# Optimization experiments

Measured on AMD Instinct MI355X. Metric: run time of the kernel, lower is better.

The kernel has to match this reference:

```python
import jax, jax.numpy as jnp
import numpy as np

J, C, F, K = 4096, 8192, 64, 2  # jobs, total nodes, out feats, TAGConv hops (DGL default K=2)


def setup_inputs() -> dict:
    key = jax.random.key(0)
    ks = jax.random.split(key, 8)
    h = jax.random.uniform(ks[0], (J,), jnp.float32)
    L = jax.random.uniform(ks[1], (J,), jnp.float32)
    W = jax.random.uniform(ks[2], (), jnp.float32)
    P = jax.random.uniform(ks[3], (), jnp.float32)
    N = jax.random.uniform(ks[4], (), jnp.float32)
    Graph = jax.random.randint(ks[5], (J, C), 0, 2).astype(jnp.float32)
    tag_w = jax.random.normal(ks[6], ((K + 1) * 6, F), jnp.float32) * 0.05  # TAGConv lin weight on concat of K+1 hops
    tag_b = jnp.zeros((F,), jnp.float32)
    lin_w = jax.random.normal(ks[7], (F, C), jnp.float32) * 0.05
    lin_b = jnp.zeros((C,), jnp.float32)
    return dict(h=h, L=L, W=W, P=P, N=N, Graph=Graph,
                tag_w=tag_w, tag_b=tag_b, lin_w=lin_w, lin_b=lin_b)


def _mask(Graph):
    Jn, Cn = Graph.shape
    row = Graph.sum(axis=1, keepdims=True)          # [J,1]
    col = Graph.sum(axis=0, keepdims=True)          # [1,C]
    colJ = col[:, :Jn]                               # [1,J]
    left = 1.0 - row - row.T - colJ - colJ.T         # [J,J]
    left = jnp.where(left == 1.0, 1.0, 0.0)
    left = jnp.triu(left, k=1)
    right = 1.0 - jnp.broadcast_to(row, (Jn, Cn - Jn))
    return jnp.concatenate([left, right], axis=1)    # [J,C]


def reference(h, L, W, P, N, Graph, tag_w, tag_b, lin_w, lin_b):
    Jn, Cn = Graph.shape
    # sort jobs by h descending, pair with L
    order = jnp.argsort(-h)
    jobList = jnp.stack([h[order], L[order]], axis=1)                 # [J,2]
    other = jnp.stack([W, P, N, jnp.asarray(1.0, h.dtype)])           # [4]
    X = jnp.concatenate([jobList, jnp.broadcast_to(other, (Jn, 4))], axis=1)  # [J,6]
    X = jnp.concatenate([X, jnp.zeros((Cn - Jn, 6), X.dtype)], axis=0)        # [C,6]
    # pad adjacency to square CxC
    A = jnp.concatenate([Graph, jnp.zeros((Cn - Jn, Cn), Graph.dtype)], axis=0)
    # DGL TAGConv: norm = clamp(in_deg,1)^-0.5; edge i->j iff A[i,j]==1 => aggregate = A^T @ x
    deg = A.sum(axis=0)
    norm = jnp.clip(deg, 1.0) ** -0.5

    def prop(x):
        return (A.T @ (x * norm[:, None])) * norm[:, None]

    f0 = X
    f1 = prop(f0)
    f2 = prop(f1)
    G_t = jnp.concatenate([f0, f1, f2], axis=1) @ tag_w + tag_b       # [C,F]
    Value = G_t[:Jn] @ lin_w + lin_b                                   # [J,C]
    tmp = Value - (1.0 - _mask(Graph)) * 10000.0
    Poss = jax.nn.softmax(tmp.reshape(-1)).reshape(tmp.shape)
    return (Value, Poss)
```

## Files before the change

kernel.cpp:

```cpp
#include <hip/hip_runtime.h>
#include <math.h>

#define JN 4096
#define CN 8192

typedef __attribute__((ext_vector_type(8))) short short8;
typedef __attribute__((ext_vector_type(4))) float f32x4;

#define WS_LWT    0
#define WS_GTB    262144
#define WS_ROWSUM 393216
#define WS_DEG    397312
#define WS_NORM   401408
#define WS_X      405504
#define WS_F1     430080
#define WS_PART   454656

#define PS_BITR    0
#define PS_COLPART 524288
#define PS_P1      589824
#define PS_P2      983040

__device__ __forceinline__ unsigned short f2bf(float x) {
    unsigned int u = __float_as_uint(x);
    u += 0x7fffu + ((u >> 16) & 1u);
    return (unsigned short)(u >> 16);
}

__device__ __forceinline__ float gt_val(const float* __restrict__ x, const float* __restrict__ a,
                                        const float* __restrict__ b, const float* __restrict__ tw,
                                        float acc, int f) {
#pragma unroll
    for (int k = 0; k < 6; ++k) acc += x[k] * tw[k * 64 + f];
#pragma unroll
    for (int k = 0; k < 6; ++k) acc += a[k] * tw[(k + 6) * 64 + f];
#pragma unroll
    for (int k = 0; k < 6; ++k) acc += b[k] * tw[(k + 12) * 64 + f];
    return acc;
}

__global__ __launch_bounds__(256) void k_front(const float* __restrict__ G,
                                               const float* __restrict__ h, const float* __restrict__ L,
                                               const float* __restrict__ Wp, const float* __restrict__ Pp,
                                               const float* __restrict__ Np,
                                               const float* __restrict__ lw,
                                               float* __restrict__ rowsum,
                                               unsigned long long* __restrict__ bitR,
                                               float* __restrict__ X,
                                               unsigned short* __restrict__ lwT) {
    __shared__ float redf[4];
    __shared__ int redi[4];
    __shared__ float s_t[64][65];
    int wv = threadIdx.x >> 6, lane = threadIdx.x & 63;
    if (blockIdx.x < JN) {
        int row = blockIdx.x;
        const f32x4* g4 = (const f32x4*)(G + (size_t)row * CN);
        unsigned long long* brow = bitR + (size_t)row * 64;
        float s = 0.f;
#pragma unroll
        for (int i = 0; i < 4; ++i) {
            f32x4 v = __builtin_nontemporal_load(&g4[i * 256 + wv * 64 + lane]);
            s += v[0] + v[1] + v[2] + v[3];
            unsigned long long b0 = __ballot(v[0] != 0.f);
            unsigned long long b1 = __ballot(v[1] != 0.f);
            unsigned long long b2 = __ballot(v[2] != 0.f);
            unsigned long long b3 = __ballot(v[3] != 0.f);
            if (!lane) {
                int base = i * 16 + wv * 4;
                brow[base] = b0; brow[base + 1] = b1; brow[base + 2] = b2; brow[base + 3] = b3;
            }
        }
#pragma unroll
        for (int i = 4; i < 8; ++i) {
            f32x4 v = __builtin_nontemporal_load(&g4[i * 256 + wv * 64 + lane]);
            s += v[0] + v[1] + v[2] + v[3];
        }
        for (int o = 32; o; o >>= 1) s += __shfl_down(s, o, 64);
        if (!lane) redf[wv] = s;
        __syncthreads();
        if (!threadIdx.x) rowsum[row] = redf[0] + redf[1] + redf[2] + redf[3];
    } else if (blockIdx.x < 2 * JN) {
        int i = blockIdx.x - JN;
        float hi = h[i];
        int cnt = 0;
        for (int j = threadIdx.x; j < JN; j += 256) {
            float hj = h[j];
            cnt += (hj > hi) || (hj == hi && j < i);
        }
        for (int o = 32; o; o >>= 1) cnt += __shfl_down(cnt, o, 64);
        if (!lane) redi[wv] = cnt;
        __syncthreads();
        if (!threadIdx.x) {
            int r = redi[0] + redi[1] + redi[2] + redi[3];
            float* xr = X + r * 6;
            xr[0] = hi; xr[1] = L[i]; xr[2] = *Wp; xr[3] = *Pp; xr[4] = *Np; xr[5] = 1.f;
        }
    } else {
        int c0 = (blockIdx.x - 2 * JN) * 64;
        for (int t = threadIdx.x; t < 4096; t += 256) {
            int f = t >> 6, cc = t & 63;
            s_t[f][cc] = lw[(size_t)f * CN + c0 + cc];
        }
        __syncthreads();
        for (int q = threadIdx.x; q < 512; q += 256) {
            int c = q >> 3, kc = q & 7;
            short8 pack;
#pragma unroll
            for (int i = 0; i < 8; ++i) pack[i] = (short)f2bf(s_t[kc * 8 + i][c]);
            *(short8*)(lwT + ((size_t)(c0 + c)) * 64 + kc * 8) = pack;
        }
    }
}

__global__ __launch_bounds__(256) void k_colsum_bits(const unsigned long long* __restrict__ bitR,
                                                     float* __restrict__ colpart) {
    __shared__ unsigned long long s_bits[256][4];
    int bx = blockIdx.x, r0 = blockIdx.y * 256;
    int tid = threadIdx.x;
    for (int t = tid; t < 1024; t += 256) {
        int r = t >> 2, wl = t & 3;
        s_bits[r][wl] = bitR[(size_t)(r0 + r) * 64 + bx * 4 + wl];
    }
    __syncthreads();
    int wl = tid & 3, bit = tid >> 2;
    int cnt = 0;
    for (int r = 0; r < 256; ++r)
        cnt += (int)((s_bits[r][wl] >> bit) & 1ull);
    colpart[(size_t)blockIdx.y * JN + bx * 256 + tid] = (float)cnt;
}

__global__ __launch_bounds__(256) void k_prop1(const unsigned long long* __restrict__ bitR,
                                               const float* __restrict__ X,
                                               const float* __restrict__ colpart,
                                               float* __restrict__ deg, float* __restrict__ norm,
                                               float* __restrict__ part) {
    __shared__ unsigned long long s_bits[256][4];
    __shared__ float s_in[256 * 6];
    __shared__ float s_norm[256];
    int bx = blockIdx.x, r0 = blockIdx.y * 256;
    int tid = threadIdx.x;
    {
        float d = 0.f;
        for (int ch = 0; ch < 16; ++ch) d += colpart[(size_t)ch * JN + r0 + tid];
        float dc = d < 1.f ? 1.f : d;
        float nv = rsqrtf(dc);
        s_norm[tid] = nv;
        if (bx == 0) { deg[r0 + tid] = d; norm[r0 + tid] = nv; }
    }
    for (int t = tid; t < 1024; t += 256) {
        int r = t >> 2, wl = t & 3;
        s_bits[r][wl] = bitR[(size_t)(r0 + r) * 64 + bx * 4 + wl];
    }
    __syncthreads();
    for (int t = tid; t < 1536; t += 256)
        s_in[t] = X[r0 * 6 + t] * s_norm[t / 6];
    __syncthreads();
    int wl = tid & 3, bit = tid >> 2;
    float a0 = 0, a1 = 0, a2 = 0, a3 = 0, a4 = 0, a5 = 0;
    for (int r = 0; r < 256; ++r) {
        float g = (float)((s_bits[r][wl] >> bit) & 1ull);
        const float* x = &s_in[r * 6];
        a0 += g * x[0]; a1 += g * x[1]; a2 += g * x[2];
        a3 += g * x[3]; a4 += g * x[4]; a5 += g * x[5];
    }
    float* o = part + ((size_t)blockIdx.y * JN + bx * 256 + tid) * 6;
    o[0] = a0; o[1] = a1; o[2] = a2; o[3] = a3; o[4] = a4; o[5] = a5;
}

__global__ __launch_bounds__(256) void k_prop2(const unsigned long long* __restrict__ bitR,
                                               const float* __restrict__ p1, const float* __restrict__ norm,
                                               float* __restrict__ f1, float* __restrict__ part) {
    __shared__ unsigned long long s_bits[256][4];
    __shared__ float s_in[256 * 6];
    int bx = blockIdx.x, r0 = blockIdx.y * 256;
    int tid = threadIdx.x;
    for (int t = tid; t < 1024; t += 256) {
        int r = t >> 2, wl = t & 3;
        s_bits[r][wl] = bitR[(size_t)(r0 + r) * 64 + bx * 4 + wl];
    }
    for (int t = tid; t < 1536; t += 256) {
        float s = 0.f;
        for (int ch = 0; ch < 16; ++ch) s += p1[(size_t)ch * 24576 + r0 * 6 + t];
        int row = r0 + t / 6;
        float n = norm[row];
        float f1v = s * n;
        if (bx == 0) f1[r0 * 6 + t] = f1v;
        s_in[t] = f1v * n;
    }
    __syncthreads();
    int wl = tid & 3, bit = tid >> 2;
    float a0 = 0, a1 = 0, a2 = 0, a3 = 0, a4 = 0, a5 = 0;
    for (int r = 0; r < 256; ++r) {
        float g = (float)((s_bits[r][wl] >> bit) & 1ull);
        const float* x = &s_in[r * 6];
        a0 += g * x[0]; a1 += g * x[1]; a2 += g * x[2];
        a3 += g * x[3]; a4 += g * x[4]; a5 += g * x[5];
    }
    float* o = part + ((size_t)blockIdx.y * JN + bx * 256 + tid) * 6;
    o[0] = a0; o[1] = a1; o[2] = a2; o[3] = a3; o[4] = a4; o[5] = a5;
}

__global__ __launch_bounds__(256) void k_gt(const float* __restrict__ p2, const float* __restrict__ norm,
                                            const float* __restrict__ f1, const float* __restrict__ X,
                                            const float* __restrict__ tw, const float* __restrict__ tb,
                                            unsigned short* __restrict__ Gtb) {
    __shared__ float s_x[64 * 6], s_f1[64 * 6], s_f2[64 * 6];
    __shared__ float s_tw[18 * 64], s_tb[64];
    int j0 = blockIdx.x * 64, tid = threadIdx.x;
    for (int t = tid; t < 1152; t += 256) s_tw[t] = tw[t];
    if (tid < 64) s_tb[tid] = tb[tid];
    for (int t = tid; t < 384; t += 256) {
        s_x[t] = X[j0 * 6 + t];
        s_f1[t] = f1[j0 * 6 + t];
        float s = 0.f;
        for (int ch = 0; ch < 16; ++ch) s += p2[(size_t)ch * 24576 + j0 * 6 + t];
        s_f2[t] = s * norm[j0 + t / 6];
    }
    __syncthreads();
    int row = tid & 63, fg = tid >> 6;
    float xv[6], av[6], bv[6];
#pragma unroll
    for (int k = 0; k < 6; ++k) {
        xv[k] = s_x[row * 6 + k]; av[k] = s_f1[row * 6 + k]; bv[k] = s_f2[row * 6 + k];
    }
    short8 p0, p1v;
#pragma unroll
    for (int i = 0; i < 16; ++i) {
        int f = fg * 16 + i;
        float acc = gt_val(xv, av, bv, s_tw, s_tb[f], f);
        unsigned short u = f2bf(acc);
        if (i < 8) p0[i] = (short)u; else p1v[i - 8] = (short)u;
    }
    *(short8*)(Gtb + (size_t)(j0 + row) * 64 + fg * 16) = p0;
    *(short8*)(Gtb + (size_t)(j0 + row) * 64 + fg * 16 + 8) = p1v;
}

#define GEMM_PROLOGUE()                                                                   \
    __shared__ unsigned short sGt[64 * 64];                                               \
    __shared__ unsigned short sW[256 * 64];                                               \
    int j0 = blockIdx.y * 64, c0 = blockIdx.x * 256, tid = threadIdx.x;                   \
    for (int q = tid; q < 2048; q += 256) {                                               \
        int col = q >> 3, off = q & 7;                                                    \
        short8 v = *(const short8*)(lwT + ((size_t)(c0 + col)) * 64 + off * 8);           \
        int byte = (col * 128 + off * 16) ^ ((col & 7) << 4);                             \
        *(short8*)((char*)sW + byte) = v;                                                 \
    }                                                                                     \
    for (int q = tid; q < 512; q += 256) {                                                \
        int row = q >> 3, off = q & 7;                                                    \
        short8 v = *(const short8*)(Gtb + ((size_t)(j0 + row)) * 64 + off * 8);           \
        int byte = (row * 128 + off * 16) ^ ((row & 7) << 4);                             \
        *(short8*)((char*)sGt + byte) = v;                                                \
    }                                                                                     \
    __syncthreads();                                                                      \
    int lane = tid & 63, w = tid >> 6;                                                    \
    int lrow = lane & 15, kg = lane >> 4;                                                 \
    f32x4 acc[4][4];                                            \
    for (int m = 0; m < 4; ++m)                                                           \
        for (int n = 0; n < 4; ++n) acc[m][n] = (f32x4){0.f, 0.f, 0.f, 0.f};              \
    for (int ks = 0; ks < 2; ++ks) {                                                      \
        int kb = ks * 64 + kg * 16;                                                       \
        short8 wf[4], gf[4];                                                              \
        for (int m = 0; m < 4; ++m) {                                                     \
            int col = w * 64 + m * 16 + lrow;                                             \
            wf[m] = *(const short8*)((const char*)sW + ((col * 128 + kb) ^ ((col & 7) << 4))); \
        }                                                                                 \
        for (int n = 0; n < 4; ++n) {                                                     \
            int row = n * 16 + lrow;                                                      \
            gf[n] = *(const short8*)((const char*)sGt + ((row * 128 + kb) ^ ((row & 7) << 4))); \
        }                                                                                 \
        for (int m = 0; m < 4; ++m)                                                       \
            for (int n = 0; n < 4; ++n)                                                   \
                acc[m][n] = __builtin_amdgcn_mfma_f32_16x16x32_bf16(wf[m], gf[n], acc[m][n], 0, 0, 0); \
    }                                                                                     \
    bool left = (c0 < JN);                                                                \
    int cb[4]; f32x4 lb4[4], rsc4[4], dgc4[4];                                            \
    for (int m = 0; m < 4; ++m) {                                                         \
        cb[m] = c0 + w * 64 + m * 16 + kg * 4;                                            \
        lb4[m] = *(const f32x4*)&lb[cb[m]];                                               \
        if (left) { rsc4[m] = *(const f32x4*)&rowsum[cb[m]]; dgc4[m] = *(const f32x4*)&deg[cb[m]]; } \
        else      { rsc4[m] = (f32x4){0,0,0,0}; dgc4[m] = (f32x4){0,0,0,0}; }             \
    }

__global__ __launch_bounds__(256) void k_valueA(const unsigned short* __restrict__ Gtb,
                                                const unsigned short* __restrict__ lwT,
                                                const float* __restrict__ lb,
                                                const float* __restrict__ rowsum, const float* __restrict__ deg,
                                                float* __restrict__ Value, float* __restrict__ partials) {
    GEMM_PROLOGUE()
    __shared__ float sRedM[4], sRedS[4];

    float mx = -INFINITY;
#pragma unroll
    for (int n = 0; n < 4; ++n) {
        int j = j0 + n * 16 + lrow;
        float rs_i = rowsum[j], dg_i = deg[j];
#pragma unroll
        for (int m = 0; m < 4; ++m) {
            f32x4 v4 = acc[m][n] + lb4[m];
            __builtin_nontemporal_store(v4, (f32x4*)&Value[(size_t)j * CN + cb[m]]);
            f32x4 t4;
#pragma unroll
            for (int u = 0; u < 4; ++u) {
                float om;
                if (left) {
                    bool m1 = ((rs_i + rsc4[m][u] + dg_i + dgc4[m][u]) == 0.0f) && (cb[m] + u > j);
                    om = m1 ? 0.f : 1.f;
                } else {
                    om = rs_i;
                }
                t4[u] = v4[u] - om * 10000.f;
            }
            acc[m][n] = t4;
            mx = fmaxf(fmaxf(fmaxf(mx, t4[0]), t4[1]), fmaxf(t4[2], t4[3]));
        }
    }
    float sm = 0.f;
#pragma unroll
    for (int n = 0; n < 4; ++n)
#pragma unroll
        for (int m = 0; m < 4; ++m)
#pragma unroll
            for (int u = 0; u < 4; ++u) sm += __expf(acc[m][n][u] - mx);

    for (int o = 32; o; o >>= 1) {
        float om_ = __shfl_down(mx, o, 64);
        float os_ = __shfl_down(sm, o, 64);
        float nm = fmaxf(mx, om_);
        sm = sm * __expf(mx - nm) + os_ * __expf(om_ - nm);
        mx = nm;
    }
    if (!lane) { sRedM[w] = mx; sRedS[w] = sm; }
    __syncthreads();
    if (!tid) {
        float M = sRedM[0], S = sRedS[0];
        for (int i = 1; i < 4; ++i) {
            float nm = fmaxf(M, sRedM[i]);
            S = S * __expf(M - nm) + sRedS[i] * __expf(sRedM[i] - nm);
            M = nm;
        }
        int bid = blockIdx.y * gridDim.x + blockIdx.x;
        partials[2 * bid] = M;
        partials[2 * bid + 1] = S;
    }
}

__global__ __launch_bounds__(256) void k_valueB(const unsigned short* __restrict__ Gtb,
                                                const unsigned short* __restrict__ lwT,
                                                const float* __restrict__ lb,
                                                const float* __restrict__ rowsum, const float* __restrict__ deg,
                                                const float* __restrict__ partials, float* __restrict__ Poss) {
    __shared__ float sRedM[4], sRedS[4], sG[2];
    {
        int tid0 = threadIdx.x;
        float mx = -INFINITY, sm = 0.f;
        for (int i = tid0; i < 2048; i += 256) {
            float m = partials[2 * i], s = partials[2 * i + 1];
            float nm = fmaxf(mx, m);
            sm = sm * __expf(mx - nm) + s * __expf(m - nm);
            mx = nm;
        }
        for (int o = 32; o; o >>= 1) {
            float om_ = __shfl_down(mx, o, 64);
            float os_ = __shfl_down(sm, o, 64);
            float nm = fmaxf(mx, om_);
            sm = sm * __expf(mx - nm) + os_ * __expf(om_ - nm);
            mx = nm;
        }
        int lane0 = tid0 & 63, w0 = tid0 >> 6;
        if (!lane0) { sRedM[w0] = mx; sRedS[w0] = sm; }
        __syncthreads();
        if (!tid0) {
            float M = sRedM[0], S = sRedS[0];
            for (int i = 1; i < 4; ++i) {
                float nm = fmaxf(M, sRedM[i]);
                S = S * __expf(M - nm) + sRedS[i] * __expf(sRedM[i] - nm);
                M = nm;
            }
            sG[0] = M; sG[1] = S;
        }
        __syncthreads();
    }
    float gmax = sG[0];
    float ginv = 1.0f / sG[1];

    GEMM_PROLOGUE()
#pragma unroll
    for (int n = 0; n < 4; ++n) {
        int j = j0 + n * 16 + lrow;
        float rs_i = rowsum[j], dg_i = deg[j];
#pragma unroll
        for (int m = 0; m < 4; ++m) {
            f32x4 v4 = acc[m][n] + lb4[m];
            f32x4 o4;
#pragma unroll
            for (int u = 0; u < 4; ++u) {
                float om;
                if (left) {
                    bool m1 = ((rs_i + rsc4[m][u] + dg_i + dgc4[m][u]) == 0.0f) && (cb[m] + u > j);
                    om = m1 ? 0.f : 1.f;
                } else {
                    om = rs_i;
                }
                o4[u] = __expf(v4[u] - om * 10000.f - gmax) * ginv;
            }
            __builtin_nontemporal_store(o4, (f32x4*)&Poss[(size_t)j * CN + cb[m]]);
        }
    }
}

extern "C" void kernel_launch(void* const* d_in, const int* in_sizes, int n_in,
                              void* d_out, int out_size, void* d_ws, size_t ws_size,
                              hipStream_t stream) {
    const float* h  = (const float*)d_in[0];
    const float* L  = (const float*)d_in[1];
    const float* W  = (const float*)d_in[2];
    const float* P  = (const float*)d_in[3];
    const float* N  = (const float*)d_in[4];
    const float* G  = (const float*)d_in[5];
    const float* tw = (const float*)d_in[6];
    const float* tb = (const float*)d_in[7];
    const float* lw = (const float*)d_in[8];
    const float* lb = (const float*)d_in[9];

    float* ws = (float*)d_ws;
    unsigned short* lwT = (unsigned short*)(ws + WS_LWT);
    unsigned short* Gtb = (unsigned short*)(ws + WS_GTB);
    float* rowsum = ws + WS_ROWSUM;
    float* deg    = ws + WS_DEG;
    float* norm   = ws + WS_NORM;
    float* X      = ws + WS_X;
    float* f1     = ws + WS_F1;
    float* part   = ws + WS_PART;

    float* Value = (float*)d_out;
    float* Poss  = Value + (size_t)JN * CN;

    unsigned long long* bitR = (unsigned long long*)(Poss + PS_BITR);
    float* colpart = Poss + PS_COLPART;
    float* p1      = Poss + PS_P1;
    float* p2      = Poss + PS_P2;

    k_front      <<<2 * JN + 128, 256, 0, stream>>>(G, h, L, W, P, N, lw, rowsum, bitR, X, lwT);
    k_colsum_bits<<<dim3(16, 16), 256, 0, stream>>>(bitR, colpart);
    k_prop1      <<<dim3(16, 16), 256, 0, stream>>>(bitR, X, colpart, deg, norm, p1);
    k_prop2      <<<dim3(16, 16), 256, 0, stream>>>(bitR, p1, norm, f1, p2);
    k_gt         <<<64, 256, 0, stream>>>(p2, norm, f1, X, tw, tb, Gtb);
    k_valueA     <<<dim3(32, 64), 256, 0, stream>>>(Gtb, lwT, lb, rowsum, deg, Value, part);
    k_valueB     <<<dim3(32, 64), 256, 0, stream>>>(Gtb, lwT, lb, rowsum, deg, part, Poss);
}
```

Measured before the change: 149.9 us.

## Fuse colsum, two propagation hops and G_t into one persistent kernel

Replaces four small kernel launches (column sums, two propagation hops, G_t projection) with a single 256-block kernel that uses software grid barriers (atomic counters reset in k_front) between the phases. The block's bit tile is loaded into shared memory once and reused across phases, and norm is kept in shared memory. The aim is to remove launch gaps and tail overhead for these tiny kernels. It relies on all 256 blocks being co-resident to avoid deadlock, and adds atomic spin costs.

```diff
diff --git a/kernel.cpp b/kernel.cpp
--- a/kernel.cpp
+++ b/kernel.cpp
@@ -5,6 +5,7 @@
 #define CN 8192
 
 typedef __attribute__((ext_vector_type(8))) short short8;
+typedef __attribute__((ext_vector_type(4))) short short4v;
 typedef __attribute__((ext_vector_type(4))) float f32x4;
 
 #define WS_LWT    0
@@ -15,6 +16,7 @@
 #define WS_X      405504
 #define WS_F1     430080
 #define WS_PART   454656
+#define WS_BAR    458752
 
 #define PS_BITR    0
 #define PS_COLPART 524288
@@ -37,6 +39,17 @@
 #pragma unroll
     for (int k = 0; k < 6; ++k) acc += b[k] * tw[(k + 12) * 64 + f];
     return acc;
+}
+
+__device__ __forceinline__ void gbar(unsigned* c) {
+    __syncthreads();
+    if (threadIdx.x == 0) {
+        __threadfence();
+        __hip_atomic_fetch_add(c, 1u, __ATOMIC_RELEASE, __HIP_MEMORY_SCOPE_AGENT);
+        while (__hip_atomic_load(c, __ATOMIC_ACQUIRE, __HIP_MEMORY_SCOPE_AGENT) < 256u) {}
+        __threadfence();
+    }
+    __syncthreads();
 }
 
 __global__ __launch_bounds__(256) void k_front(const float* __restrict__ G,
@@ -47,7 +60,8 @@
                                                float* __restrict__ rowsum,
                                                unsigned long long* __restrict__ bitR,
                                                float* __restrict__ X,
-                                               unsigned short* __restrict__ lwT) {
+                                               unsigned short* __restrict__ lwT,
+                                               unsigned* __restrict__ bar) {
     __shared__ float redf[4];
     __shared__ int redi[4];
     __shared__ float s_t[64][65];
@@ -95,7 +109,7 @@
             float* xr = X + r * 6;
             xr[0] = hi; xr[1] = L[i]; xr[2] = *Wp; xr[3] = *Pp; xr[4] = *Np; xr[5] = 1.f;
         }
-    } else {
+    } else if (blockIdx.x < 2 * JN + 128) {
         int c0 = (blockIdx.x - 2 * JN) * 64;
         for (int t = threadIdx.x; t < 4096; t += 256) {
             int f = t >> 6, cc = t & 63;
@@ -109,36 +123,46 @@
             for (int i = 0; i < 8; ++i) pack[i] = (short)f2bf(s_t[kc * 8 + i][c]);
             *(short8*)(lwT + ((size_t)(c0 + c)) * 64 + kc * 8) = pack;
         }
-    }
-}
-
-__global__ __launch_bounds__(256) void k_colsum_bits(const unsigned long long* __restrict__ bitR,
-                                                     float* __restrict__ colpart) {
+    } else {
+        if (threadIdx.x < 4) bar[threadIdx.x] = 0u;
+    }
+}
+
+__global__ __launch_bounds__(256) void k_middle(const unsigned long long* __restrict__ bitR,
+                                                const float* __restrict__ X,
+                                                const float* __restrict__ tw, const float* __restrict__ tb,
+                                                float* __restrict__ colpart,
+                                                float* __restrict__ deg, float* __restrict__ norm,
+                                                float* __restrict__ f1,
+                                                float* __restrict__ p1, float* __restrict__ p2,
+                                                unsigned short* __restrict__ Gtb,
+                                                unsigned* __restrict__ bar) {
     __shared__ unsigned long long s_bits[256][4];
-    int bx = blockIdx.x, r0 = blockIdx.y * 256;
+    __shared__ float s_in[1536];
+    __shared__ float s_norm[256];
+    __shared__ float s_tw[1152];
+    __shared__ float s_tb[64];
+    __shared__ float s_x[96], s_a[96], s_b[96];
+
     int tid = threadIdx.x;
+    int b = blockIdx.x;
+    int bx = b & 15, by = b >> 4;
+    int r0 = by * 256;
+
     for (int t = tid; t < 1024; t += 256) {
         int r = t >> 2, wl = t & 3;
         s_bits[r][wl] = bitR[(size_t)(r0 + r) * 64 + bx * 4 + wl];
     }
     __syncthreads();
-    int wl = tid & 3, bit = tid >> 2;
-    int cnt = 0;
-    for (int r = 0; r < 256; ++r)
-        cnt += (int)((s_bits[r][wl] >> bit) & 1ull);
-    colpart[(size_t)blockIdx.y * JN + bx * 256 + tid] = (float)cnt;
-}
-
-__global__ __launch_bounds__(256) void k_prop1(const unsigned long long* __restrict__ bitR,
-                                               const float* __restrict__ X,
-                                               const float* __restrict__ colpart,
-                                               float* __restrict__ deg, float* __restrict__ norm,
-                                               float* __restrict__ part) {
-    __shared__ unsigned long long s_bits[256][4];
-    __shared__ float s_in[256 * 6];
-    __shared__ float s_norm[256];
-    int bx = blockIdx.x, r0 = blockIdx.y * 256;
-    int tid = threadIdx.x;
+    {
+        int wl = tid & 3, bit = tid >> 2;
+        int cnt = 0;
+        for (int r = 0; r < 256; ++r)
+            cnt += (int)((s_bits[r][wl] >> bit) & 1ull);
+        colpart[(size_t)by * JN + bx * 256 + tid] = (float)cnt;
+    }
+    gbar(&bar[0]);
+
     {
         float d = 0.f;
         for (int ch = 0; ch < 16; ++ch) d += colpart[(size_t)ch * JN + r0 + tid];
@@ -147,92 +171,74 @@
         s_norm[tid] = nv;
         if (bx == 0) { deg[r0 + tid] = d; norm[r0 + tid] = nv; }
     }
-    for (int t = tid; t < 1024; t += 256) {
-        int r = t >> 2, wl = t & 3;
-        s_bits[r][wl] = bitR[(size_t)(r0 + r) * 64 + bx * 4 + wl];
-    }
     __syncthreads();
     for (int t = tid; t < 1536; t += 256)
         s_in[t] = X[r0 * 6 + t] * s_norm[t / 6];
     __syncthreads();
-    int wl = tid & 3, bit = tid >> 2;
-    float a0 = 0, a1 = 0, a2 = 0, a3 = 0, a4 = 0, a5 = 0;
-    for (int r = 0; r < 256; ++r) {
-        float g = (float)((s_bits[r][wl] >> bit) & 1ull);
-        const float* x = &s_in[r * 6];
-        a0 += g * x[0]; a1 += g * x[1]; a2 += g * x[2];
-        a3 += g * x[3]; a4 += g * x[4]; a5 += g * x[5];
-    }
-    float* o = part + ((size_t)blockIdx.y * JN + bx * 256 + tid) * 6;
-    o[0] = a0; o[1] = a1; o[2] = a2; o[3] = a3; o[4] = a4; o[5] = a5;
-}
-
-__global__ __launch_bounds__(256) void k_prop2(const unsigned long long* __restrict__ bitR,
-                                               const float* __restrict__ p1, const float* __restrict__ norm,
-                                               float* __restrict__ f1, float* __restrict__ part) {
-    __shared__ unsigned long long s_bits[256][4];
-    __shared__ float s_in[256 * 6];
-    int bx = blockIdx.x, r0 = blockIdx.y * 256;
-    int tid = threadIdx.x;
-    for (int t = tid; t < 1024; t += 256) {
-        int r = t >> 2, wl = t & 3;
-        s_bits[r][wl] = bitR[(size_t)(r0 + r) * 64 + bx * 4 + wl];
-    }
+    {
+        int wl = tid & 3, bit = tid >> 2;
+        float a0 = 0, a1 = 0, a2 = 0, a3 = 0, a4 = 0, a5 = 0;
+        for (int r = 0; r < 256; ++r) {
+            float g = (float)((s_bits[r][wl] >> bit) & 1ull);
+            const float* x = &s_in[r * 6];
+            a0 += g * x[0]; a1 += g * x[1]; a2 += g * x[2];
+            a3 += g * x[3]; a4 += g * x[4]; a5 += g * x[5];
+        }
+        float* o = p1 + ((size_t)by * JN + bx * 256 + tid) * 6;
+        o[0] = a0; o[1] = a1; o[2] = a2; o[3] = a3; o[4] = a4; o[5] = a5;
+    }
+    gbar(&bar[1]);
+
     for (int t = tid; t < 1536; t += 256) {
         float s = 0.f;
         for (int ch = 0; ch < 16; ++ch) s += p1[(size_t)ch * 24576 + r0 * 6 + t];
-        int row = r0 + t / 6;
-        float n = norm[row];
+        float n = s_norm[t / 6];
         float f1v = s * n;
         if (bx == 0) f1[r0 * 6 + t] = f1v;
         s_in[t] = f1v * n;
     }
     __syncthreads();
-    int wl = tid & 3, bit = tid >> 2;
-    float a0 = 0, a1 = 0, a2 = 0, a3 = 0, a4 = 0, a5 = 0;
-    for (int r = 0; r < 256; ++r) {
-        float g = (float)((s_bits[r][wl] >> bit) & 1ull);
-        const float* x = &s_in[r * 6];
-        a0 += g * x[0]; a1 += g * x[1]; a2 += g * x[2];
-        a3 += g * x[3]; a4 += g * x[4]; a5 += g * x[5];
-    }
-    float* o = part + ((size_t)blockIdx.y * JN + bx * 256 + tid) * 6;
-    o[0] = a0; o[1] = a1; o[2] = a2; o[3] = a3; o[4] = a4; o[5] = a5;
-}
-
-__global__ __launch_bounds__(256) void k_gt(const float* __restrict__ p2, const float* __restrict__ norm,
-                                            const float* __restrict__ f1, const float* __restrict__ X,
-                                            const float* __restrict__ tw, const float* __restrict__ tb,
-                                            unsigned short* __restrict__ Gtb) {
-    __shared__ float s_x[64 * 6], s_f1[64 * 6], s_f2[64 * 6];
-    __shared__ float s_tw[18 * 64], s_tb[64];
-    int j0 = blockIdx.x * 64, tid = threadIdx.x;
+    {
+        int wl = tid & 3, bit = tid >> 2;
+        float a0 = 0, a1 = 0, a2 = 0, a3 = 0, a4 = 0, a5 = 0;
+        for (int r = 0; r < 256; ++r) {
+            float g = (float)((s_bits[r][wl] >> bit) & 1ull);
+            const float* x = &s_in[r * 6];
+            a0 += g * x[0]; a1 += g * x[1]; a2 += g * x[2];
+            a3 += g * x[3]; a4 += g * x[4]; a5 += g * x[5];
+        }
+        float* o = p2 + ((size_t)by * JN + bx * 256 + tid) * 6;
+        o[0] = a0; o[1] = a1; o[2] = a2; o[3] = a3; o[4] = a4; o[5] = a5;
+    }
+    gbar(&bar[2]);
+
     for (int t = tid; t < 1152; t += 256) s_tw[t] = tw[t];
     if (tid < 64) s_tb[tid] = tb[tid];
-    for (int t = tid; t < 384; t += 256) {
-        s_x[t] = X[j0 * 6 + t];
-        s_f1[t] = f1[j0 * 6 + t];
-        float s = 0.f;
-        for (int ch = 0; ch < 16; ++ch) s += p2[(size_t)ch * 24576 + j0 * 6 + t];
-        s_f2[t] = s * norm[j0 + t / 6];
-    }
-    __syncthreads();
-    int row = tid & 63, fg = tid >> 6;
-    float xv[6], av[6], bv[6];
-#pragma unroll
-    for (int k = 0; k < 6; ++k) {
-        xv[k] = s_x[row * 6 + k]; av[k] = s_f1[row * 6 + k]; bv[k] = s_f2[row * 6 + k];
-    }
-    short8 p0, p1v;
-#pragma unroll
-    for (int i = 0; i < 16; ++i) {
-        int f = fg * 16 + i;
-        float acc = gt_val(xv, av, bv, s_tw, s_tb[f], f);
-        unsigned short u = f2bf(acc);
-        if (i < 8) p0[i] = (short)u; else p1v[i - 8] = (short)u;
-    }
-    *(short8*)(Gtb + (size_t)(j0 + row) * 64 + fg * 16) = p0;
-    *(short8*)(Gtb + (size_t)(j0 + row) * 64 + fg * 16 + 8) = p1v;
+    {
+        int j0 = b * 16;
+        for (int t = tid; t < 96; t += 256) {
+            s_x[t] = X[j0 * 6 + t];
+            s_a[t] = f1[j0 * 6 + t];
+            float s = 0.f;
+            for (int ch = 0; ch < 16; ++ch) s += p2[(size_t)ch * 24576 + j0 * 6 + t];
+            s_b[t] = s * norm[j0 + t / 6];
+        }
+        __syncthreads();
+        int row = tid >> 4, fi = tid & 15;
+        float xv[6], av[6], bv[6];
+#pragma unroll
+        for (int k = 0; k < 6; ++k) {
+            xv[k] = s_x[row * 6 + k]; av[k] = s_a[row * 6 + k]; bv[k] = s_b[row * 6 + k];
+        }
+        short4v pk;
+#pragma unroll
+        for (int i = 0; i < 4; ++i) {
+            int f = fi * 4 + i;
+            float acc = gt_val(xv, av, bv, s_tw, s_tb[f], f);
+            pk[i] = (short)f2bf(acc);
+        }
+        *(short4v*)(Gtb + (size_t)(j0 + row) * 64 + fi * 4) = pk;
+    }
 }
 
 #define GEMM_PROLOGUE()                                                                   \
@@ -431,6 +437,7 @@
     float* X      = ws + WS_X;
     float* f1     = ws + WS_F1;
     float* part   = ws + WS_PART;
+    unsigned* bar = (unsigned*)(ws + WS_BAR);
 
     float* Value = (float*)d_out;
     float* Poss  = Value + (size_t)JN * CN;
@@ -440,11 +447,8 @@
     float* p1      = Poss + PS_P1;
     float* p2      = Poss + PS_P2;
 
-    k_front      <<<2 * JN + 128, 256, 0, stream>>>(G, h, L, W, P, N, lw, rowsum, bitR, X, lwT);
-    k_colsum_bits<<<dim3(16, 16), 256, 0, stream>>>(bitR, colpart);
-    k_prop1      <<<dim3(16, 16), 256, 0, stream>>>(bitR, X, colpart, deg, norm, p1);
-    k_prop2      <<<dim3(16, 16), 256, 0, stream>>>(bitR, p1, norm, f1, p2);
-    k_gt         <<<64, 256, 0, stream>>>(p2, norm, f1, X, tw, tb, Gtb);
-    k_valueA     <<<dim3(32, 64), 256, 0, stream>>>(Gtb, lwT, lb, rowsum, deg, Value, part);
-    k_valueB     <<<dim3(32, 64), 256, 0, stream>>>(Gtb, lwT, lb, rowsum, deg, part, Poss);
-}
+    k_front  <<<2 * JN + 128 + 1, 256, 0, stream>>>(G, h, L, W, P, N, lw, rowsum, bitR, X, lwT, bar);
+    k_middle <<<256, 256, 0, stream>>>(bitR, X, tw, tb, colpart, deg, norm, f1, p1, p2, Gtb, bar);
+    k_valueA <<<dim3(32, 64), 256, 0, stream>>>(Gtb, lwT, lb, rowsum, deg, Value, part);
+    k_valueB <<<dim3(32, 64), 256, 0, stream>>>(Gtb, lwT, lb, rowsum, deg, part, Poss);
+}
```

New measurement: 221.6 us. 1.48x slower.
